# Performance work log

Measured on AMD Instinct MI355X. Metric: run time of the kernel, lower is better.

## Reference

```python
import jax, jax.numpy as jnp
import numpy as np

B, S, D, K = 8, 2048, 1024, 204  # K = int(0.1 * seq_len)
LN_EPS = 1e-12


def setup_inputs() -> dict:
    key = jax.random.key(0)
    ks = jax.random.split(key, 8)
    scale = 0.02
    return {
        "input_tensor": jax.random.normal(ks[0], (B, S, D), jnp.float32),
        "attention_mask": jnp.zeros((B, 1, 1, S), jnp.float32),  # unused by module
        "Wq": jax.random.normal(ks[1], (D, K), jnp.float32) * scale,
        "bq": jnp.zeros((K,), jnp.float32),
        "Wk": jax.random.normal(ks[2], (D, K), jnp.float32) * scale,
        "bk": jnp.zeros((K,), jnp.float32),
        "Wv": jax.random.normal(ks[3], (D, D), jnp.float32) * scale,
        "bv": jnp.zeros((D,), jnp.float32),
        "Wd": jax.random.normal(ks[4], (D, D), jnp.float32) * scale,
        "bd": jnp.zeros((D,), jnp.float32),
        "gamma": jnp.ones((D,), jnp.float32),
        "beta": jnp.zeros((D,), jnp.float32),
    }


def reference(input_tensor, attention_mask, Wq, bq, Wk, bk, Wv, bv, Wd, bd, gamma, beta):
    # factorized synthesizer: low-rank (k=204) Q/K projections
    q = input_tensor @ Wq + bq          # [B,S,K]
    k = input_tensor @ Wk + bk          # [B,S,K]
    v = input_tensor @ Wv + bv          # [B,S,D]
    scores = jnp.einsum('bsk,btk->bst', q, k)          # [B,S,S]
    probs = jax.nn.softmax(scores, axis=-1)
    # per-head matmul with broadcast probs == direct matmul on merged heads
    ctx = jnp.einsum('bst,btd->bsd', probs, v)          # [B,S,D]
    h = ctx @ Wd + bd
    y = h + input_tensor                                 # residual
    mean = jnp.mean(y, axis=-1, keepdims=True)
    var = jnp.mean(jnp.square(y - mean), axis=-1, keepdims=True)
    return gamma * (y - mean) / jnp.sqrt(var + LN_EPS) + beta
```

## Files before the change

kernel.cpp:

```cpp
#include <hip/hip_runtime.h>
#include <stdint.h>

#define BB 8
#define SS 2048
#define DD 1024
#define KREAL 204
#define KP 256
#define BM 128
#define BK 64

typedef __attribute__((ext_vector_type(8))) short short8;
typedef __attribute__((ext_vector_type(4))) float floatx4;
typedef uint16_t u16;
typedef uint32_t u32;

__device__ __forceinline__ float bf2f(u16 u) {
    union { float f; u32 i; } c; c.i = ((u32)u) << 16; return c.f;
}
__device__ __forceinline__ u16 f2bf(float f) {
    union { float f; u32 i; } c; c.f = f;
    u32 i = c.i;
    u32 r = (i + 0x7FFFu + ((i >> 16) & 1u)) >> 16;
    return (u16)r;
}

union V16 { uint4 u; short8 s8; u16 h[8]; };

#if defined(__has_builtin)
#if __has_builtin(__builtin_amdgcn_global_load_lds)
#define HAVE_GLL 1
#endif
#endif

__device__ __forceinline__ void gload16(const u16* g, u16* l) {
#ifdef HAVE_GLL
    __builtin_amdgcn_global_load_lds(
        (const __attribute__((address_space(1))) void*)(uintptr_t)g,
        (__attribute__((address_space(3))) void*)(u32)(uintptr_t)(void*)l,
        16, 0, 0);
#else
    *(uint4*)l = *(const uint4*)g;
#endif
}

__device__ __forceinline__ void stage128(const u16* __restrict__ src, size_t ld,
                                         u16* lds, int tid) {
#pragma unroll
    for (int j = 0; j < 4; j++) {
        int flat = j * 256 + tid;
        int row = flat >> 3, slot = flat & 7;
        int kg = slot ^ (row & 7);
        gload16(src + (size_t)row * ld + kg * 8, lds + flat * 8);
    }
}
__device__ __forceinline__ void stage64(const u16* __restrict__ src, size_t ld,
                                        u16* lds, int tid) {
#pragma unroll
    for (int j = 0; j < 2; j++) {
        int flat = j * 256 + tid;
        int row = flat >> 3, slot = flat & 7;
        int kg = slot ^ (row & 7);
        gload16(src + (size_t)row * ld + kg * 8, lds + flat * 8);
    }
}

__device__ __forceinline__ short8 frag(const u16* lds, int row, int kslot) {
    return *(const short8*)&lds[(row << 6) + (((kslot ^ (row & 7)) & 7) << 3)];
}

__device__ __forceinline__ void mfma_step(const u16* As, const u16* Bs,
                                          int wm, int wn, int ln, int quad,
                                          floatx4 acc[4][4]) {
#pragma unroll
    for (int kk = 0; kk < 2; kk++) {
        short8 av[4], bv[4];
#pragma unroll
        for (int mt = 0; mt < 4; mt++) av[mt] = frag(As, wm * 64 + mt * 16 + ln, kk * 4 + quad);
#pragma unroll
        for (int nt = 0; nt < 4; nt++) bv[nt] = frag(Bs, wn * 64 + nt * 16 + ln, kk * 4 + quad);
#pragma unroll
        for (int mt = 0; mt < 4; mt++)
#pragma unroll
            for (int nt = 0; nt < 4; nt++)
                acc[mt][nt] = __builtin_amdgcn_mfma_f32_16x16x32_bf16(av[mt], bv[nt], acc[mt][nt], 0, 0, 0);
    }
}

template <typename F>
__device__ __forceinline__ void store_rowmajor_128(
    u16* smem, u16* gbase, size_t ldc, int wm, int quad, int ln, int wn,
    int tid, F valfn) {
    for (int half = 0; half < 2; half++) {
        __syncthreads();
        if (wm == half) {
#pragma unroll
            for (int mt = 0; mt < 4; mt++)
#pragma unroll
                for (int nt = 0; nt < 4; nt++)
#pragma unroll
                    for (int r = 0; r < 4; r++)
                        smem[(mt * 16 + quad * 4 + r) * 136 + wn * 64 + nt * 16 + ln] =
                            valfn(mt, nt, r);
        }
        __syncthreads();
#pragma unroll
        for (int it = 0; it < 4; it++) {
            int g = it * 256 + tid;
            int row = g >> 4, tch = g & 15;
            uint4 v = *(const uint4*)&smem[row * 136 + tch * 8];
            *(uint4*)&gbase[(size_t)(half * 64 + row) * ldc + tch * 8] = v;
        }
    }
}

template <typename F4>
__device__ __forceinline__ void store_transposed_128(
    u16* smem, u16* gbase, size_t ldg, int wm, int wn, int ln, int quad,
    int tid, F4 valfn4) {
    for (int half = 0; half < 2; half++) {
        __syncthreads();
        if (wn == half) {
#pragma unroll
            for (int mt = 0; mt < 4; mt++)
#pragma unroll
                for (int nt = 0; nt < 4; nt++) {
                    ushort4 v = valfn4(mt, nt);
                    *(ushort4*)&smem[(nt * 16 + ln) * 136 + wm * 64 + mt * 16 + quad * 4] = v;
                }
        }
        __syncthreads();
#pragma unroll
        for (int it = 0; it < 4; it++) {
            int g = it * 256 + tid;
            int c = g >> 4, sch = g & 15;
            uint4 v = *(const uint4*)&smem[c * 136 + sch * 8];
            *(uint4*)&gbase[(size_t)(half * 64 + c) * ldg + sch * 8] = v;
        }
    }
}

__global__ __launch_bounds__(256) void k_cast_bf16(
    const float* __restrict__ x, u16* __restrict__ o) {
    size_t i = ((size_t)blockIdx.x * 256 + threadIdx.x) * 4;
    float4 v = *(const float4*)&x[i];
    ushort4 p;
    p.x = f2bf(v.x); p.y = f2bf(v.y); p.z = f2bf(v.z); p.w = f2bf(v.w);
    *(ushort4*)&o[i] = p;
}

__global__ __launch_bounds__(256) void k_prep(
    const float* __restrict__ Wq, const float* __restrict__ Wk,
    const float* __restrict__ Wv, const float* __restrict__ Wd,
    const float* __restrict__ bv, const float* __restrict__ bd,
    const float* __restrict__ bq, const float* __restrict__ bk,
    u16* __restrict__ Wqkt, u16* __restrict__ Wv16, u16* __restrict__ Wdt,
    float* __restrict__ bc, float* __restrict__ bqk) {
    const int z = blockIdx.z;
    const int t = threadIdx.x;
    if (z == 4) {
        int id = blockIdx.y * 32 + blockIdx.x;
        if (id < 16) {
            __shared__ float red[4][64];
            int n = id * 64 + (t & 63);
            int dc = t >> 6;
            float s = 0.f;
            for (int d = dc * 256; d < dc * 256 + 256; d++)
                s += bv[d] * Wd[(size_t)d * 1024 + n];
            red[dc][t & 63] = s;
            __syncthreads();
            if (dc == 0) bc[n] = bd[n] + red[0][t & 63] + red[1][t & 63] + red[2][t & 63] + red[3][t & 63];
        } else if (id == 16) {
            for (int i = t; i < 512; i += 256) {
                float v = 0.f;
                if (i < KREAL) v = bq[i];
                else if (i >= 256 && i < 256 + KREAL) v = bk[i - 256];
                bqk[i] = v;
            }
        }
        return;
    }
    __shared__ u16 tile[32][33];
    int k0 = blockIdx.x * 32, n0 = blockIdx.y * 32;
    int tx = t & 31, ty = t >> 5;
    if (z == 2) {
        for (int i = ty; i < 32; i += 8) {
            size_t idx = (size_t)(k0 + i) * 1024 + n0 + tx;
            Wv16[idx] = f2bf(Wv[idx]);
        }
        return;
    }
    const float* W; u16* out; int N, Npad, rowoff;
    if (z == 0)      { W = Wq; out = Wqkt; N = KREAL; Npad = 256;  rowoff = 0;   }
    else if (z == 1) { W = Wk; out = Wqkt; N = KREAL; Npad = 256;  rowoff = 256; }
    else             { W = Wd; out = Wdt;  N = 1024;  Npad = 1024; rowoff = 0;   }
    if (n0 >= Npad) return;
    for (int i = ty; i < 32; i += 8) {
        int n = n0 + tx;
        tile[i][tx] = (n < N) ? f2bf(W[(size_t)(k0 + i) * N + n]) : (u16)0;
    }
    __syncthreads();
    for (int i = ty; i < 32; i += 8) {
        int n = n0 + i;
        if (n < Npad) out[(size_t)(rowoff + n) * 1024 + k0 + tx] = tile[tx][i];
    }
}

__global__ __launch_bounds__(256) void k_gemm64(
    const u16* __restrict__ A, const u16* __restrict__ Bt,
    u16* __restrict__ C, int ldc) {
    __shared__ u16 As[64 * 64];
    __shared__ u16 Bs[64 * 64];
    const int tid = threadIdx.x;
    const int m0 = blockIdx.x * 64, n0 = blockIdx.y * 64;
    const int lane = tid & 63, w = tid >> 6;
    const int ln = lane & 15, quad = lane >> 4;

    floatx4 acc[4];
    floatx4 zero = {0.f, 0.f, 0.f, 0.f};
#pragma unroll
    for (int nt = 0; nt < 4; nt++) acc[nt] = zero;

    for (int kt = 0; kt < 16; kt++) {
        __syncthreads();
        stage64(A + (size_t)m0 * 1024 + kt * 64, 1024, As, tid);
        stage64(Bt + (size_t)n0 * 1024 + kt * 64, 1024, Bs, tid);
        __syncthreads();
#pragma unroll
        for (int kk = 0; kk < 2; kk++) {
            short8 av = frag(As, w * 16 + ln, kk * 4 + quad);
#pragma unroll
            for (int nt = 0; nt < 4; nt++) {
                short8 bvf = frag(Bs, nt * 16 + ln, kk * 4 + quad);
                acc[nt] = __builtin_amdgcn_mfma_f32_16x16x32_bf16(av, bvf, acc[nt], 0, 0, 0);
            }
        }
    }
    const int row0 = m0 + w * 16 + quad * 4;
#pragma unroll
    for (int nt = 0; nt < 4; nt++) {
        const int col = n0 + nt * 16 + ln;
        ushort4 pk;
        pk.x = f2bf(acc[nt][0]); pk.y = f2bf(acc[nt][1]);
        pk.z = f2bf(acc[nt][2]); pk.w = f2bf(acc[nt][3]);
        *reinterpret_cast<ushort4*>(&C[(size_t)col * ldc + row0]) = pk;
    }
}

__global__ __launch_bounds__(256) void k_proj(
    const u16* __restrict__ A, const u16* __restrict__ Wqkt,
    const u16* __restrict__ Wvdt, const float* __restrict__ bqk,
    u16* __restrict__ qkp, u16* __restrict__ ut) {
    __shared__ u16 smem[2 * BM * BK];
    u16* As = smem; u16* Bs = smem + BM * BK;
    const int tid = threadIdx.x;
    const int m0 = blockIdx.x * BM;
    const int by = blockIdx.y;
    const int lane = tid & 63, w = tid >> 6;
    const int wm = w >> 1, wn = w & 1;
    const int ln = lane & 15, quad = lane >> 4;

    const int n0 = (by < 4) ? by * 128 : (by - 4) * 128;
    const u16* Bb = (by < 4) ? (Wqkt + (size_t)n0 * 1024) : (Wvdt + (size_t)n0 * 1024);

    floatx4 acc[4][4];
    floatx4 zero = {0.f, 0.f, 0.f, 0.f};
#pragma unroll
    for (int mt = 0; mt < 4; mt++)
#pragma unroll
        for (int nt = 0; nt < 4; nt++) acc[mt][nt] = zero;

    const u16* Ab = A + (size_t)m0 * 1024;
    for (int kt = 0; kt < 16; kt++) {
        __syncthreads();
        stage128(Ab + kt * BK, 1024, As, tid);
        stage128(Bb + kt * BK, 1024, Bs, tid);
        __syncthreads();
        mfma_step(As, Bs, wm, wn, ln, quad, acc);
    }

    if (by < 4) {
        u16* gbase = qkp + (size_t)m0 * 512 + n0;
        store_rowmajor_128(smem, gbase, 512, wm, quad, ln, wn, tid,
            [&](int mt, int nt, int r) -> u16 {
                int col = n0 + wn * 64 + nt * 16 + ln;
                return f2bf(acc[mt][nt][r] + bqk[col]);
            });
    } else {
        int b = m0 >> 11, s0loc = m0 & 2047;
        u16* gbase = ut + ((size_t)b * DD + n0) * SS + s0loc;
        store_transposed_128(smem, gbase, SS, wm, wn, ln, quad, tid,
            [&](int mt, int nt) -> ushort4 {
                ushort4 pk;
                pk.x = f2bf(acc[mt][nt][0]); pk.y = f2bf(acc[mt][nt][1]);
                pk.z = f2bf(acc[mt][nt][2]); pk.w = f2bf(acc[mt][nt][3]);
                return pk;
            });
    }
}

__global__ __launch_bounds__(256) void k_gemm_qk(
    const u16* __restrict__ qkp, u16* __restrict__ P, float* __restrict__ lg) {
    __shared__ u16 smem[2 * BM * BK];
    u16* As = smem; u16* Bs = smem + BM * BK;
    const int tid = threadIdx.x;
    const int s0 = blockIdx.x * BM, t0 = blockIdx.y * BM, bb = blockIdx.z;
    const int lane = tid & 63, w = tid >> 6;
    const int wm = w >> 1, wn = w & 1;
    const int ln = lane & 15, quad = lane >> 4;

    floatx4 acc[4][4];
    floatx4 zero = {0.f, 0.f, 0.f, 0.f};
#pragma unroll
    for (int mt = 0; mt < 4; mt++)
#pragma unroll
        for (int nt = 0; nt < 4; nt++) acc[mt][nt] = zero;

    const u16* Ab = qkp + ((size_t)bb * SS + s0) * 512;
    const u16* Bb = qkp + ((size_t)bb * SS + t0) * 512 + 256;
#pragma unroll
    for (int kt = 0; kt < KP / BK; kt++) {
        __syncthreads();
        stage128(Ab + kt * BK, 512, As, tid);
        stage128(Bb + kt * BK, 512, Bs, tid);
        __syncthreads();
        mfma_step(As, Bs, wm, wn, ln, quad, acc);
    }

#pragma unroll
    for (int mt = 0; mt < 4; mt++) {
        const int row0 = s0 + wm * 64 + mt * 16 + quad * 4;
#pragma unroll
        for (int r = 0; r < 4; r++) {
            float rs = __expf(acc[mt][0][r] - 30.f) + __expf(acc[mt][1][r] - 30.f)
                     + __expf(acc[mt][2][r] - 30.f) + __expf(acc[mt][3][r] - 30.f);
            rs += __shfl_xor(rs, 1);
            rs += __shfl_xor(rs, 2);
            rs += __shfl_xor(rs, 4);
            rs += __shfl_xor(rs, 8);
            if (ln == 0) atomicAdd(&lg[bb * SS + row0 + r], rs);
        }
    }

    u16* gbase = P + (size_t)bb * SS * SS + (size_t)s0 * SS + t0;
    store_rowmajor_128(smem, gbase, SS, wm, quad, ln, wn, tid,
        [&](int mt, int nt, int r) -> u16 {
            return f2bf(__expf(acc[mt][nt][r] - 30.f));
        });
}

__global__ __launch_bounds__(256) void k_gemm_h(
    const u16* __restrict__ P, const u16* __restrict__ ut,
    const float* __restrict__ lg, const float* __restrict__ bc,
    const float* __restrict__ xres, u16* __restrict__ y) {
    __shared__ u16 smem[2 * BM * BK];
    u16* As = smem; u16* Bs = smem + BM * BK;
    const int tid = threadIdx.x;
    const int s0 = blockIdx.x * BM, d0 = blockIdx.y * BM, bb = blockIdx.z;
    const int lane = tid & 63, w = tid >> 6;
    const int wm = w >> 1, wn = w & 1;
    const int ln = lane & 15, quad = lane >> 4;

    floatx4 acc[4][4];
    floatx4 zero = {0.f, 0.f, 0.f, 0.f};
#pragma unroll
    for (int mt = 0; mt < 4; mt++)
#pragma unroll
        for (int nt = 0; nt < 4; nt++) acc[mt][nt] = zero;

    const u16* Ab = P + ((size_t)bb * SS + s0) * SS;
    const u16* Bb = ut + ((size_t)bb * DD + d0) * SS;
    for (int kt = 0; kt < SS / BK; kt++) {
        __syncthreads();
        stage128(Ab + kt * BK, SS, As, tid);
        stage128(Bb + kt * BK, SS, Bs, tid);
        __syncthreads();
        mfma_step(As, Bs, wm, wn, ln, quad, acc);
    }

    u16* gbase = y + ((size_t)bb * SS + s0) * DD + d0;
    store_rowmajor_128(smem, gbase, DD, wm, quad, ln, wn, tid,
        [&](int mt, int nt, int r) -> u16 {
            int rowl = wm * 64 + mt * 16 + quad * 4 + r;
            size_t grow = (size_t)bb * SS + s0 + rowl;
            int col = d0 + wn * 64 + nt * 16 + ln;
            float inv = 1.f / lg[grow];
            return f2bf(acc[mt][nt][r] * inv + bc[col] + xres[grow * DD + col]);
        });
}

__global__ __launch_bounds__(256) void k_layernorm(
    const u16* __restrict__ y, const float* __restrict__ gamma,
    const float* __restrict__ beta, float* __restrict__ out) {
    const int tid = threadIdx.x;
    const int lane = tid & 63, w = tid >> 6;
    const size_t row = (size_t)blockIdx.x * 4 + w;
    const u16* yr = y + row * DD;

    float v[16];
#pragma unroll
    for (int j = 0; j < 2; j++) {
        V16 t;
        t.u = *(const uint4*)&yr[j * 512 + lane * 8];
#pragma unroll
        for (int e = 0; e < 8; e++) v[j * 8 + e] = bf2f(t.h[e]);
    }
    float s = 0.f, sq = 0.f;
#pragma unroll
    for (int i = 0; i < 16; i++) { s += v[i]; sq += v[i] * v[i]; }
#pragma unroll
    for (int msk = 1; msk < 64; msk <<= 1) {
        s  += __shfl_xor(s,  msk, 64);
        sq += __shfl_xor(sq, msk, 64);
    }
    float mean = s * (1.f / 1024.f);
    float var  = sq * (1.f / 1024.f) - mean * mean;
    float rstd = rsqrtf(fmaxf(var, 0.f) + 1e-12f);
#pragma unroll
    for (int j = 0; j < 2; j++) {
        int cbase = j * 512 + lane * 8;
#pragma unroll
        for (int h = 0; h < 2; h++) {
            float4 g  = *(const float4*)&gamma[cbase + h * 4];
            float4 bt = *(const float4*)&beta [cbase + h * 4];
            float4 o;
            o.x = g.x * (v[j * 8 + h * 4 + 0] - mean) * rstd + bt.x;
            o.y = g.y * (v[j * 8 + h * 4 + 1] - mean) * rstd + bt.y;
            o.z = g.z * (v[j * 8 + h * 4 + 2] - mean) * rstd + bt.z;
            o.w = g.w * (v[j * 8 + h * 4 + 3] - mean) * rstd + bt.w;
            *(float4*)&out[row * DD + cbase + h * 4] = o;
        }
    }
}

extern "C" void kernel_launch(void* const* d_in, const int* in_sizes, int n_in,
                              void* d_out, int out_size, void* d_ws, size_t ws_size,
                              hipStream_t stream) {
    const float* x     = (const float*)d_in[0];
    const float* Wq    = (const float*)d_in[2];
    const float* bq    = (const float*)d_in[3];
    const float* Wk    = (const float*)d_in[4];
    const float* bk    = (const float*)d_in[5];
    const float* Wv    = (const float*)d_in[6];
    const float* bv    = (const float*)d_in[7];
    const float* Wd    = (const float*)d_in[8];
    const float* bd    = (const float*)d_in[9];
    const float* gamma = (const float*)d_in[10];
    const float* beta  = (const float*)d_in[11];
    float* out = (float*)d_out;

    char* ws = (char*)d_ws;
    u16*   qkp  = (u16*)(ws + 0);
    u16*   ut   = (u16*)(ws + (16u << 20));
    u16*   x16  = (u16*)(ws + (48u << 20));
    u16*   P    = (u16*)(ws + (48u << 20));
    u16*   Wv16 = (u16*)(ws + (80u << 20));
    u16*   Wvdt = (u16*)(ws + (80u << 20) + 2097152);
    u16*   y    = (u16*)(ws + (80u << 20));
    float* lg   = (float*)(ws + 117440512);
    float* bc   = (float*)(ws + 117506048);
    float* bqk  = (float*)(ws + 117510144);
    u16*   Wqkt = (u16*)(ws + 117512192);
    u16*   Wdt  = (u16*)(ws + 118560768);

    dim3 blk(256);

    k_cast_bf16<<<dim3(16384), blk, 0, stream>>>(x, x16);
    k_prep<<<dim3(32, 32, 5), blk, 0, stream>>>(Wq, Wk, Wv, Wd, bv, bd, bq, bk,
                                                Wqkt, Wv16, Wdt, bc, bqk);

    k_gemm64<<<dim3(16, 16), blk, 0, stream>>>(Wv16, Wdt, Wvdt, 1024);

    k_proj<<<dim3(128, 12), blk, 0, stream>>>(x16, Wqkt, Wvdt, bqk, qkp, ut);

    hipMemsetAsync(lg, 0, (size_t)BB * SS * sizeof(float), stream);

    for (int g = 0; g < 2; g++) {
        const size_t qo = (size_t)g * 4 * SS * 512;
        const size_t uo = (size_t)g * 4 * (size_t)DD * SS;
        const size_t yo = (size_t)g * 4 * (size_t)SS * DD;
        const size_t lo = (size_t)g * 4 * SS;
        k_gemm_qk<<<dim3(16, 16, 4), blk, 0, stream>>>(qkp + qo, P, lg + lo);
        k_gemm_h <<<dim3(16, 8, 4),  blk, 0, stream>>>(P, ut + uo, lg + lo, bc, x + yo, y + yo);
    }

    k_layernorm<<<dim3(4096), blk, 0, stream>>>(y, gamma, beta, out);
}
```

Measured before the change: 381.3 us.

## Use pipelined 256x256 MFMA GEMM core with 512-thread blocks across all batches

Replaces the 128x128 single-buffered GEMM loop with a 256x256-tile core that prefetches K-slices into rotating LDS planes. It uses raw vmcnt waits and barriers and raises wave priority around the MFMA bursts, so global loads overlap compute and each staged tile is reused more. The QK and PV kernels now cover all 8 batches in one launch each instead of two groups of four. The PV epilogue writes fp32 residual sums straight into the output, and layernorm runs in place, which removes the bf16 y round-trip. The costs are larger LDS per block, higher register pressure, fewer blocks in flight, and a workspace layout where the full P buffer overlaps the weight scratch areas that are no longer needed by then.

```diff
diff --git a/kernel.cpp b/kernel.cpp
--- a/kernel.cpp
+++ b/kernel.cpp
@@ -5,9 +5,6 @@
 #define SS 2048
 #define DD 1024
 #define KREAL 204
-#define KP 256
-#define BM 128
-#define BK 64
 
 typedef __attribute__((ext_vector_type(8))) short short8;
 typedef __attribute__((ext_vector_type(4))) float floatx4;
@@ -23,8 +20,6 @@
     u32 r = (i + 0x7FFFu + ((i >> 16) & 1u)) >> 16;
     return (u16)r;
 }
-
-union V16 { uint4 u; short8 s8; u16 h[8]; };
 
 #if defined(__has_builtin)
 #if __has_builtin(__builtin_amdgcn_global_load_lds)
@@ -43,16 +38,9 @@
 #endif
 }
 
-__device__ __forceinline__ void stage128(const u16* __restrict__ src, size_t ld,
-                                         u16* lds, int tid) {
-#pragma unroll
-    for (int j = 0; j < 4; j++) {
-        int flat = j * 256 + tid;
-        int row = flat >> 3, slot = flat & 7;
-        int kg = slot ^ (row & 7);
-        gload16(src + (size_t)row * ld + kg * 8, lds + flat * 8);
-    }
-}
+#define VM_WAIT(N) asm volatile("s_waitcnt vmcnt(" #N ")" ::: "memory")
+#define S_BAR()    asm volatile("s_barrier" ::: "memory")
+
 __device__ __forceinline__ void stage64(const u16* __restrict__ src, size_t ld,
                                         u16* lds, int tid) {
 #pragma unroll
@@ -63,78 +51,178 @@
         gload16(src + (size_t)row * ld + kg * 8, lds + flat * 8);
     }
 }
-
 __device__ __forceinline__ short8 frag(const u16* lds, int row, int kslot) {
     return *(const short8*)&lds[(row << 6) + (((kslot ^ (row & 7)) & 7) << 3)];
 }
 
-__device__ __forceinline__ void mfma_step(const u16* As, const u16* Bs,
-                                          int wm, int wn, int ln, int quad,
-                                          floatx4 acc[4][4]) {
-#pragma unroll
-    for (int kk = 0; kk < 2; kk++) {
-        short8 av[4], bv[4];
-#pragma unroll
-        for (int mt = 0; mt < 4; mt++) av[mt] = frag(As, wm * 64 + mt * 16 + ln, kk * 4 + quad);
-#pragma unroll
-        for (int nt = 0; nt < 4; nt++) bv[nt] = frag(Bs, wn * 64 + nt * 16 + ln, kk * 4 + quad);
-#pragma unroll
-        for (int mt = 0; mt < 4; mt++)
-#pragma unroll
-            for (int nt = 0; nt < 4; nt++)
-                acc[mt][nt] = __builtin_amdgcn_mfma_f32_16x16x32_bf16(av[mt], bv[nt], acc[mt][nt], 0, 0, 0);
+__device__ __forceinline__ short8 frag32(const u16* plane, int row, int ks) {
+    return *(const short8*)&plane[(row << 5) + (((ks ^ ((row >> 1) & 3)) & 3) << 3)];
+}
+
+__device__ __forceinline__ void stage_half(const u16* s0, const u16* s1,
+                                           u16* dp, int tid) {
+    gload16(s0, dp + tid * 8);
+    gload16(s1, dp + 4096 + tid * 8);
+}
+
+template <int MT, bool LOADB>
+__device__ __forceinline__ void phase16(const u16* Apl, const u16* Bpl,
+                                        int arow, int brow, int ln, int quad,
+                                        short8 (&bv)[4], floatx4 (&acc)[8][4]) {
+    short8 af[4];
+#pragma unroll
+    for (int i = 0; i < 4; i++) af[i] = frag32(Apl, arow + (MT + i) * 16 + ln, quad);
+    if (LOADB) {
+#pragma unroll
+        for (int nt = 0; nt < 4; nt++) bv[nt] = frag32(Bpl, brow + nt * 16 + ln, quad);
+    }
+    __builtin_amdgcn_s_setprio(1);
+#pragma unroll
+    for (int i = 0; i < 4; i++)
+#pragma unroll
+        for (int nt = 0; nt < 4; nt++)
+            acc[MT + i][nt] = __builtin_amdgcn_mfma_f32_16x16x32_bf16(
+                af[i], bv[nt], acc[MT + i][nt], 0, 0, 0);
+    __builtin_amdgcn_s_setprio(0);
+}
+
+template <int NT>
+__device__ __forceinline__ void gemm_core256(
+    const u16* __restrict__ Ag, size_t lda,
+    const u16* __restrict__ Bg, size_t ldb,
+    u16* lds, int tid, floatx4 (&acc)[8][4]) {
+    const int lane = tid & 63, w = tid >> 6;
+    const int arow = (w >> 2) * 128, brow = (w & 3) * 64;
+    const int ln = lane & 15, quad = lane >> 4;
+    const int srow = tid >> 2;
+    const int kgp = (tid & 3) ^ ((srow >> 1) & 3);
+    const u16* A0 = Ag + (size_t)srow * lda + kgp * 8;
+    const u16* A1 = Ag + (size_t)(srow + 128) * lda + kgp * 8;
+    const u16* B0 = Bg + (size_t)srow * ldb + kgp * 8;
+    const u16* B1 = Bg + (size_t)(srow + 128) * ldb + kgp * 8;
+    u16* Al = lds;
+    u16* Bl = lds + 32768;
+
+    stage_half(A0,      A1,      Al,         tid);
+    stage_half(B0,      B1,      Bl,         tid);
+    stage_half(A0 + 32, A1 + 32, Al + 8192,  tid);
+    stage_half(B0 + 32, B1 + 32, Bl + 8192,  tid);
+    stage_half(A0 + 64, A1 + 64, Al + 16384, tid);
+    stage_half(B0 + 64, B1 + 64, Bl + 16384, tid);
+
+    short8 bv[4];
+#pragma unroll 2
+    for (int t = 0; t < NT - 1; ++t) {
+        const int p  = (t & 1) * 2;
+        const int pn = 2 - p;
+        const u16* Ap0 = Al + p * 8192;
+        const u16* Ap1 = Al + p * 8192 + 8192;
+        const u16* Bp0 = Bl + p * 8192;
+        const u16* Bp1 = Bl + p * 8192 + 8192;
+        const size_t o1 = (size_t)(t + 1) * 64;
+        const size_t o2 = (size_t)(t + 2) * 64;
+        VM_WAIT(8); S_BAR();
+        stage_half(A0 + o1 + 32, A1 + o1 + 32, Al + (pn + 1) * 8192, tid);
+        phase16<0, true >(Ap0, Bp0, arow, brow, ln, quad, bv, acc);
+        stage_half(B0 + o1 + 32, B1 + o1 + 32, Bl + (pn + 1) * 8192, tid);
+        phase16<4, false>(Ap0, Bp0, arow, brow, ln, quad, bv, acc);
+        VM_WAIT(8); S_BAR();
+        if (t + 2 < NT) stage_half(A0 + o2, A1 + o2, Al + p * 8192, tid);
+        phase16<0, true >(Ap1, Bp1, arow, brow, ln, quad, bv, acc);
+        if (t + 2 < NT) stage_half(B0 + o2, B1 + o2, Bl + p * 8192, tid);
+        phase16<4, false>(Ap1, Bp1, arow, brow, ln, quad, bv, acc);
+    }
+    {
+        const int p = ((NT - 1) & 1) * 2;
+        const u16* Ap0 = Al + p * 8192;
+        const u16* Ap1 = Al + p * 8192 + 8192;
+        const u16* Bp0 = Bl + p * 8192;
+        const u16* Bp1 = Bl + p * 8192 + 8192;
+        VM_WAIT(4); S_BAR();
+        phase16<0, true >(Ap0, Bp0, arow, brow, ln, quad, bv, acc);
+        phase16<4, false>(Ap0, Bp0, arow, brow, ln, quad, bv, acc);
+        VM_WAIT(0); S_BAR();
+        phase16<0, true >(Ap1, Bp1, arow, brow, ln, quad, bv, acc);
+        phase16<4, false>(Ap1, Bp1, arow, brow, ln, quad, bv, acc);
     }
 }
 
 template <typename F>
-__device__ __forceinline__ void store_rowmajor_128(
-    u16* smem, u16* gbase, size_t ldc, int wm, int quad, int ln, int wn,
-    int tid, F valfn) {
+__device__ __forceinline__ void store_rm256(u16* smem, u16* gbase, size_t ldc,
+                                            int wm, int wn, int ln, int quad,
+                                            int tid, F val) {
     for (int half = 0; half < 2; half++) {
         __syncthreads();
         if (wm == half) {
 #pragma unroll
-            for (int mt = 0; mt < 4; mt++)
+            for (int mt = 0; mt < 8; mt++)
 #pragma unroll
                 for (int nt = 0; nt < 4; nt++)
 #pragma unroll
                     for (int r = 0; r < 4; r++)
-                        smem[(mt * 16 + quad * 4 + r) * 136 + wn * 64 + nt * 16 + ln] =
-                            valfn(mt, nt, r);
-        }
-        __syncthreads();
-#pragma unroll
-        for (int it = 0; it < 4; it++) {
-            int g = it * 256 + tid;
-            int row = g >> 4, tch = g & 15;
-            uint4 v = *(const uint4*)&smem[row * 136 + tch * 8];
-            *(uint4*)&gbase[(size_t)(half * 64 + row) * ldc + tch * 8] = v;
+                        smem[(mt * 16 + quad * 4 + r) * 264 + wn * 64 + nt * 16 + ln] =
+                            val(mt, nt, r);
+        }
+        __syncthreads();
+#pragma unroll
+        for (int j = 0; j < 8; j++) {
+            int flat = j * 512 + tid;
+            int row = flat >> 5, c = flat & 31;
+            *(uint4*)&gbase[(size_t)(half * 128 + row) * ldc + c * 8] =
+                *(const uint4*)&smem[row * 264 + c * 8];
         }
     }
 }
 
 template <typename F4>
-__device__ __forceinline__ void store_transposed_128(
-    u16* smem, u16* gbase, size_t ldg, int wm, int wn, int ln, int quad,
-    int tid, F4 valfn4) {
-    for (int half = 0; half < 2; half++) {
-        __syncthreads();
-        if (wn == half) {
-#pragma unroll
-            for (int mt = 0; mt < 4; mt++)
+__device__ __forceinline__ void store_tr256(u16* smem, u16* gbase, size_t ldg,
+                                            int wm, int wn, int ln, int quad,
+                                            int tid, F4 val4) {
+    for (int qr = 0; qr < 4; qr++) {
+        __syncthreads();
+        if (wn == qr) {
+#pragma unroll
+            for (int mt = 0; mt < 8; mt++)
 #pragma unroll
                 for (int nt = 0; nt < 4; nt++) {
-                    ushort4 v = valfn4(mt, nt);
-                    *(ushort4*)&smem[(nt * 16 + ln) * 136 + wm * 64 + mt * 16 + quad * 4] = v;
+                    ushort4 v = val4(mt, nt);
+                    *(ushort4*)&smem[(nt * 16 + ln) * 264 + wm * 128 + mt * 16 + quad * 4] = v;
                 }
         }
         __syncthreads();
 #pragma unroll
-        for (int it = 0; it < 4; it++) {
-            int g = it * 256 + tid;
-            int c = g >> 4, sch = g & 15;
-            uint4 v = *(const uint4*)&smem[c * 136 + sch * 8];
-            *(uint4*)&gbase[(size_t)(half * 64 + c) * ldg + sch * 8] = v;
+        for (int j = 0; j < 4; j++) {
+            int flat = j * 512 + tid;
+            int c = flat >> 5, r8 = flat & 31;
+            *(uint4*)&gbase[(size_t)(qr * 64 + c) * ldg + r8 * 8] =
+                *(const uint4*)&smem[c * 264 + r8 * 8];
+        }
+    }
+}
+
+template <typename F>
+__device__ __forceinline__ void store_rm256_f32(float* smem, float* gbase, size_t ldc,
+                                                int wm, int wn, int ln, int quad,
+                                                int tid, F val) {
+    for (int c4 = 0; c4 < 4; c4++) {
+        __syncthreads();
+        if (wm == (c4 >> 1)) {
+#pragma unroll
+            for (int i = 0; i < 4; i++)
+#pragma unroll
+                for (int nt = 0; nt < 4; nt++)
+#pragma unroll
+                    for (int r = 0; r < 4; r++)
+                        smem[(i * 16 + quad * 4 + r) * 260 + wn * 64 + nt * 16 + ln] =
+                            val((c4 & 1) * 4 + i, nt, r);
+        }
+        __syncthreads();
+#pragma unroll
+        for (int j = 0; j < 8; j++) {
+            int flat = j * 512 + tid;
+            int row = flat >> 6, q = flat & 63;
+            *(float4*)&gbase[(size_t)(c4 * 64 + row) * ldc + q * 4] =
+                *(const float4*)&smem[row * 260 + q * 4];
         }
     }
 }
@@ -246,49 +334,41 @@
     }
 }
 
-__global__ __launch_bounds__(256) void k_proj(
+__global__ __launch_bounds__(512, 2) void k_proj2(
     const u16* __restrict__ A, const u16* __restrict__ Wqkt,
     const u16* __restrict__ Wvdt, const float* __restrict__ bqk,
     u16* __restrict__ qkp, u16* __restrict__ ut) {
-    __shared__ u16 smem[2 * BM * BK];
-    u16* As = smem; u16* Bs = smem + BM * BK;
+    __shared__ __align__(16) u16 lds[65536];
     const int tid = threadIdx.x;
-    const int m0 = blockIdx.x * BM;
+    const int m0 = blockIdx.x * 256;
     const int by = blockIdx.y;
     const int lane = tid & 63, w = tid >> 6;
-    const int wm = w >> 1, wn = w & 1;
+    const int wm = w >> 2, wn = w & 3;
     const int ln = lane & 15, quad = lane >> 4;
 
-    const int n0 = (by < 4) ? by * 128 : (by - 4) * 128;
-    const u16* Bb = (by < 4) ? (Wqkt + (size_t)n0 * 1024) : (Wvdt + (size_t)n0 * 1024);
-
-    floatx4 acc[4][4];
+    floatx4 acc[8][4];
     floatx4 zero = {0.f, 0.f, 0.f, 0.f};
 #pragma unroll
-    for (int mt = 0; mt < 4; mt++)
+    for (int mt = 0; mt < 8; mt++)
 #pragma unroll
         for (int nt = 0; nt < 4; nt++) acc[mt][nt] = zero;
 
-    const u16* Ab = A + (size_t)m0 * 1024;
-    for (int kt = 0; kt < 16; kt++) {
-        __syncthreads();
-        stage128(Ab + kt * BK, 1024, As, tid);
-        stage128(Bb + kt * BK, 1024, Bs, tid);
-        __syncthreads();
-        mfma_step(As, Bs, wm, wn, ln, quad, acc);
-    }
-
-    if (by < 4) {
-        u16* gbase = qkp + (size_t)m0 * 512 + n0;
-        store_rowmajor_128(smem, gbase, 512, wm, quad, ln, wn, tid,
+    const u16* Ag = A + (size_t)m0 * 1024;
+    const int n0 = (by < 2) ? by * 256 : (by - 2) * 256;
+    const u16* Bg = (by < 2) ? (Wqkt + (size_t)n0 * 1024) : (Wvdt + (size_t)n0 * 1024);
+    gemm_core256<16>(Ag, 1024, Bg, 1024, lds, tid, acc);
+
+    if (by < 2) {
+        float b4[4];
+#pragma unroll
+        for (int nt = 0; nt < 4; nt++) b4[nt] = bqk[n0 + wn * 64 + nt * 16 + ln];
+        store_rm256(lds, qkp + (size_t)m0 * 512 + n0, 512, wm, wn, ln, quad, tid,
             [&](int mt, int nt, int r) -> u16 {
-                int col = n0 + wn * 64 + nt * 16 + ln;
-                return f2bf(acc[mt][nt][r] + bqk[col]);
+                return f2bf(acc[mt][nt][r] + b4[nt]);
             });
     } else {
         int b = m0 >> 11, s0loc = m0 & 2047;
-        u16* gbase = ut + ((size_t)b * DD + n0) * SS + s0loc;
-        store_transposed_128(smem, gbase, SS, wm, wn, ln, quad, tid,
+        store_tr256(lds, ut + ((size_t)b * DD + n0) * SS + s0loc, SS, wm, wn, ln, quad, tid,
             [&](int mt, int nt) -> ushort4 {
                 ushort4 pk;
                 pk.x = f2bf(acc[mt][nt][0]); pk.y = f2bf(acc[mt][nt][1]);
@@ -298,111 +378,105 @@
     }
 }
 
-__global__ __launch_bounds__(256) void k_gemm_qk(
+__global__ __launch_bounds__(512, 2) void k_qk2(
     const u16* __restrict__ qkp, u16* __restrict__ P, float* __restrict__ lg) {
-    __shared__ u16 smem[2 * BM * BK];
-    u16* As = smem; u16* Bs = smem + BM * BK;
+    __shared__ __align__(16) u16 lds[65536];
     const int tid = threadIdx.x;
-    const int s0 = blockIdx.x * BM, t0 = blockIdx.y * BM, bb = blockIdx.z;
+    const int s0 = blockIdx.x * 256, t0 = blockIdx.y * 256, bb = blockIdx.z;
     const int lane = tid & 63, w = tid >> 6;
-    const int wm = w >> 1, wn = w & 1;
+    const int wm = w >> 2, wn = w & 3;
     const int ln = lane & 15, quad = lane >> 4;
 
-    floatx4 acc[4][4];
+    floatx4 acc[8][4];
     floatx4 zero = {0.f, 0.f, 0.f, 0.f};
 #pragma unroll
-    for (int mt = 0; mt < 4; mt++)
+    for (int mt = 0; mt < 8; mt++)
 #pragma unroll
         for (int nt = 0; nt < 4; nt++) acc[mt][nt] = zero;
 
-    const u16* Ab = qkp + ((size_t)bb * SS + s0) * 512;
-    const u16* Bb = qkp + ((size_t)bb * SS + t0) * 512 + 256;
-#pragma unroll
-    for (int kt = 0; kt < KP / BK; kt++) {
-        __syncthreads();
-        stage128(Ab + kt * BK, 512, As, tid);
-        stage128(Bb + kt * BK, 512, Bs, tid);
-        __syncthreads();
-        mfma_step(As, Bs, wm, wn, ln, quad, acc);
-    }
-
-#pragma unroll
-    for (int mt = 0; mt < 4; mt++) {
-        const int row0 = s0 + wm * 64 + mt * 16 + quad * 4;
+    gemm_core256<4>(qkp + ((size_t)bb * SS + s0) * 512, 512,
+                    qkp + ((size_t)bb * SS + t0) * 512 + 256, 512, lds, tid, acc);
+
+#pragma unroll
+    for (int mt = 0; mt < 8; mt++)
+#pragma unroll
+        for (int nt = 0; nt < 4; nt++)
+#pragma unroll
+            for (int r = 0; r < 4; r++)
+                acc[mt][nt][r] = __expf(acc[mt][nt][r] - 30.f);
+
+#pragma unroll
+    for (int mt = 0; mt < 8; mt++) {
 #pragma unroll
         for (int r = 0; r < 4; r++) {
-            float rs = __expf(acc[mt][0][r] - 30.f) + __expf(acc[mt][1][r] - 30.f)
-                     + __expf(acc[mt][2][r] - 30.f) + __expf(acc[mt][3][r] - 30.f);
+            float rs = acc[mt][0][r] + acc[mt][1][r] + acc[mt][2][r] + acc[mt][3][r];
             rs += __shfl_xor(rs, 1);
             rs += __shfl_xor(rs, 2);
             rs += __shfl_xor(rs, 4);
             rs += __shfl_xor(rs, 8);
-            if (ln == 0) atomicAdd(&lg[bb * SS + row0 + r], rs);
-        }
-    }
-
-    u16* gbase = P + (size_t)bb * SS * SS + (size_t)s0 * SS + t0;
-    store_rowmajor_128(smem, gbase, SS, wm, quad, ln, wn, tid,
-        [&](int mt, int nt, int r) -> u16 {
-            return f2bf(__expf(acc[mt][nt][r] - 30.f));
-        });
-}
-
-__global__ __launch_bounds__(256) void k_gemm_h(
+            if (ln == 0)
+                atomicAdd(&lg[(size_t)bb * SS + s0 + wm * 128 + mt * 16 + quad * 4 + r], rs);
+        }
+    }
+
+    store_rm256(lds, P + (size_t)bb * SS * SS + (size_t)s0 * SS + t0, SS,
+                wm, wn, ln, quad, tid,
+        [&](int mt, int nt, int r) -> u16 { return f2bf(acc[mt][nt][r]); });
+}
+
+__global__ __launch_bounds__(512, 2) void k_h2(
     const u16* __restrict__ P, const u16* __restrict__ ut,
     const float* __restrict__ lg, const float* __restrict__ bc,
-    const float* __restrict__ xres, u16* __restrict__ y) {
-    __shared__ u16 smem[2 * BM * BK];
-    u16* As = smem; u16* Bs = smem + BM * BK;
+    const float* __restrict__ xres, float* __restrict__ out) {
+    __shared__ __align__(16) u16 lds[65536];
     const int tid = threadIdx.x;
-    const int s0 = blockIdx.x * BM, d0 = blockIdx.y * BM, bb = blockIdx.z;
+    const int s0 = blockIdx.x * 256, d0 = blockIdx.y * 256, bb = blockIdx.z;
     const int lane = tid & 63, w = tid >> 6;
-    const int wm = w >> 1, wn = w & 1;
+    const int wm = w >> 2, wn = w & 3;
     const int ln = lane & 15, quad = lane >> 4;
 
-    floatx4 acc[4][4];
+    floatx4 acc[8][4];
     floatx4 zero = {0.f, 0.f, 0.f, 0.f};
 #pragma unroll
-    for (int mt = 0; mt < 4; mt++)
+    for (int mt = 0; mt < 8; mt++)
 #pragma unroll
         for (int nt = 0; nt < 4; nt++) acc[mt][nt] = zero;
 
-    const u16* Ab = P + ((size_t)bb * SS + s0) * SS;
-    const u16* Bb = ut + ((size_t)bb * DD + d0) * SS;
-    for (int kt = 0; kt < SS / BK; kt++) {
-        __syncthreads();
-        stage128(Ab + kt * BK, SS, As, tid);
-        stage128(Bb + kt * BK, SS, Bs, tid);
-        __syncthreads();
-        mfma_step(As, Bs, wm, wn, ln, quad, acc);
-    }
-
-    u16* gbase = y + ((size_t)bb * SS + s0) * DD + d0;
-    store_rowmajor_128(smem, gbase, DD, wm, quad, ln, wn, tid,
-        [&](int mt, int nt, int r) -> u16 {
-            int rowl = wm * 64 + mt * 16 + quad * 4 + r;
-            size_t grow = (size_t)bb * SS + s0 + rowl;
+    gemm_core256<32>(P + ((size_t)bb * SS + s0) * SS, SS,
+                     ut + ((size_t)bb * DD + d0) * SS, SS, lds, tid, acc);
+
+    float b4[4];
+#pragma unroll
+    for (int nt = 0; nt < 4; nt++) b4[nt] = bc[d0 + wn * 64 + nt * 16 + ln];
+    float inv[8][4];
+#pragma unroll
+    for (int mt = 0; mt < 8; mt++)
+#pragma unroll
+        for (int r = 0; r < 4; r++)
+            inv[mt][r] = 1.f / lg[(size_t)bb * SS + s0 + wm * 128 + mt * 16 + quad * 4 + r];
+
+    store_rm256_f32((float*)lds, out + ((size_t)bb * SS + s0) * DD + d0, DD,
+                    wm, wn, ln, quad, tid,
+        [&](int mt, int nt, int r) -> float {
+            size_t grow = (size_t)bb * SS + s0 + wm * 128 + mt * 16 + quad * 4 + r;
             int col = d0 + wn * 64 + nt * 16 + ln;
-            float inv = 1.f / lg[grow];
-            return f2bf(acc[mt][nt][r] * inv + bc[col] + xres[grow * DD + col]);
+            return acc[mt][nt][r] * inv[mt][r] + b4[nt] + xres[grow * DD + col];
         });
 }
 
-__global__ __launch_bounds__(256) void k_layernorm(
-    const u16* __restrict__ y, const float* __restrict__ gamma,
-    const float* __restrict__ beta, float* __restrict__ out) {
+__global__ __launch_bounds__(256) void k_ln_f32(
+    float* __restrict__ io, const float* __restrict__ gamma,
+    const float* __restrict__ beta) {
     const int tid = threadIdx.x;
     const int lane = tid & 63, w = tid >> 6;
     const size_t row = (size_t)blockIdx.x * 4 + w;
-    const u16* yr = y + row * DD;
+    float* rp = io + row * DD;
 
     float v[16];
 #pragma unroll
-    for (int j = 0; j < 2; j++) {
-        V16 t;
-        t.u = *(const uint4*)&yr[j * 512 + lane * 8];
-#pragma unroll
-        for (int e = 0; e < 8; e++) v[j * 8 + e] = bf2f(t.h[e]);
+    for (int j = 0; j < 4; j++) {
+        float4 t = *(const float4*)&rp[j * 256 + lane * 4];
+        v[j * 4 + 0] = t.x; v[j * 4 + 1] = t.y; v[j * 4 + 2] = t.z; v[j * 4 + 3] = t.w;
     }
     float s = 0.f, sq = 0.f;
 #pragma unroll
@@ -416,19 +490,15 @@
     float var  = sq * (1.f / 1024.f) - mean * mean;
     float rstd = rsqrtf(fmaxf(var, 0.f) + 1e-12f);
 #pragma unroll
-    for (int j = 0; j < 2; j++) {
-        int cbase = j * 512 + lane * 8;
-#pragma unroll
-        for (int h = 0; h < 2; h++) {
-            float4 g  = *(const float4*)&gamma[cbase + h * 4];
-            float4 bt = *(const float4*)&beta [cbase + h * 4];
-            float4 o;
-            o.x = g.x * (v[j * 8 + h * 4 + 0] - mean) * rstd + bt.x;
-            o.y = g.y * (v[j * 8 + h * 4 + 1] - mean) * rstd + bt.y;
-            o.z = g.z * (v[j * 8 + h * 4 + 2] - mean) * rstd + bt.z;
-            o.w = g.w * (v[j * 8 + h * 4 + 3] - mean) * rstd + bt.w;
-            *(float4*)&out[row * DD + cbase + h * 4] = o;
-        }
+    for (int j = 0; j < 4; j++) {
+        float4 g  = *(const float4*)&gamma[j * 256 + lane * 4];
+        float4 bt = *(const float4*)&beta [j * 256 + lane * 4];
+        float4 o;
+        o.x = g.x * (v[j * 4 + 0] - mean) * rstd + bt.x;
+        o.y = g.y * (v[j * 4 + 1] - mean) * rstd + bt.y;
+        o.z = g.z * (v[j * 4 + 2] - mean) * rstd + bt.z;
+        o.w = g.w * (v[j * 4 + 3] - mean) * rstd + bt.w;
+        *(float4*)&rp[j * 256 + lane * 4] = o;
     }
 }
 
@@ -450,38 +520,28 @@
 
     char* ws = (char*)d_ws;
     u16*   qkp  = (u16*)(ws + 0);
-    u16*   ut   = (u16*)(ws + (16u << 20));
-    u16*   x16  = (u16*)(ws + (48u << 20));
-    u16*   P    = (u16*)(ws + (48u << 20));
-    u16*   Wv16 = (u16*)(ws + (80u << 20));
-    u16*   Wvdt = (u16*)(ws + (80u << 20) + 2097152);
-    u16*   y    = (u16*)(ws + (80u << 20));
+    u16*   ut   = (u16*)(ws + 16777216);
+    u16*   P    = (u16*)(ws + 50331648);
+    u16*   x16  = (u16*)(ws + 50331648);
+    u16*   Wv16 = (u16*)(ws + 83886080);
+    u16*   Wvdt = (u16*)(ws + 85983232);
+    u16*   Wdt  = (u16*)(ws + 88080384);
+    u16*   Wqkt = (u16*)(ws + 90177536);
     float* lg   = (float*)(ws + 117440512);
     float* bc   = (float*)(ws + 117506048);
     float* bqk  = (float*)(ws + 117510144);
-    u16*   Wqkt = (u16*)(ws + 117512192);
-    u16*   Wdt  = (u16*)(ws + 118560768);
-
-    dim3 blk(256);
-
-    k_cast_bf16<<<dim3(16384), blk, 0, stream>>>(x, x16);
-    k_prep<<<dim3(32, 32, 5), blk, 0, stream>>>(Wq, Wk, Wv, Wd, bv, bd, bq, bk,
-                                                Wqkt, Wv16, Wdt, bc, bqk);
-
-    k_gemm64<<<dim3(16, 16), blk, 0, stream>>>(Wv16, Wdt, Wvdt, 1024);
-
-    k_proj<<<dim3(128, 12), blk, 0, stream>>>(x16, Wqkt, Wvdt, bqk, qkp, ut);
+
+    k_cast_bf16<<<dim3(16384), dim3(256), 0, stream>>>(x, x16);
+    k_prep<<<dim3(32, 32, 5), dim3(256), 0, stream>>>(Wq, Wk, Wv, Wd, bv, bd, bq, bk,
+                                                      Wqkt, Wv16, Wdt, bc, bqk);
+    k_gemm64<<<dim3(16, 16), dim3(256), 0, stream>>>(Wv16, Wdt, Wvdt, 1024);
+
+    k_proj2<<<dim3(64, 6), dim3(512), 0, stream>>>(x16, Wqkt, Wvdt, bqk, qkp, ut);
 
     hipMemsetAsync(lg, 0, (size_t)BB * SS * sizeof(float), stream);
 
-    for (int g = 0; g < 2; g++) {
-        const size_t qo = (size_t)g * 4 * SS * 512;
-        const size_t uo = (size_t)g * 4 * (size_t)DD * SS;
-        const size_t yo = (size_t)g * 4 * (size_t)SS * DD;
-        const size_t lo = (size_t)g * 4 * SS;
-        k_gemm_qk<<<dim3(16, 16, 4), blk, 0, stream>>>(qkp + qo, P, lg + lo);
-        k_gemm_h <<<dim3(16, 8, 4),  blk, 0, stream>>>(P, ut + uo, lg + lo, bc, x + yo, y + yo);
-    }
-
-    k_layernorm<<<dim3(4096), blk, 0, stream>>>(y, gamma, beta, out);
-}
+    k_qk2<<<dim3(8, 8, 8), dim3(512), 0, stream>>>(qkp, P, lg);
+    k_h2 <<<dim3(8, 4, 8), dim3(512), 0, stream>>>(P, ut, lg, bc, x, out);
+
+    k_ln_f32<<<dim3(4096), dim3(256), 0, stream>>>(out, gamma, beta);
+}
```

Measured after the change: 361.7 us. -5.1%, faster.
